# Kernel tuning notes

Hardware: AMD Instinct MI355X
Metric: run time of the kernel (lower is better)

Reference implementation:

```python
import jax, jax.numpy as jnp
import numpy as np

N_USER, N_ITEM, D = 50000, 100000, 64
E_UI, E_UU = 1000000, 800000
NEG_SLOPE = 0.2


def gatv2(x_src, x_dst, src_idx, dst_idx, w_src, w_dst, attn, bias, n_dst):
    """DGL GATv2Conv, num_heads=1: e = a . leaky_relu(Ws x_u + Wd x_v),
    segment-softmax over edges incoming to each dst node, message = Ws x_u."""
    hs = x_src @ w_src                      # [Ns, D]
    hd = x_dst @ w_dst                      # [Nd, D]
    pre = jax.nn.leaky_relu(hs[src_idx] + hd[dst_idx], NEG_SLOPE)  # [E, D]
    e = pre @ attn                          # [E]
    emax = jax.ops.segment_max(e, dst_idx, num_segments=n_dst)     # -inf for empty
    a = jnp.exp(e - emax[dst_idx])          # [E]
    denom = jax.ops.segment_sum(a, dst_idx, num_segments=n_dst)    # [Nd]
    num = jax.ops.segment_sum(hs[src_idx] * a[:, None], dst_idx, num_segments=n_dst)
    out = num / jnp.maximum(denom, 1e-9)[:, None]
    return out + bias


def setup_inputs() -> dict:
    key = jax.random.key(0)
    ks = jax.random.split(key, 32)
    s = 1.0 / np.sqrt(D)
    def W(k):
        return jax.random.normal(k, (D, D), jnp.float32) * s
    inp = {
        "h_user": jax.random.normal(ks[0], (N_USER, D), jnp.float32),
        "h_item": jax.random.normal(ks[1], (N_ITEM, D), jnp.float32),
        "rate_src": jax.random.randint(ks[2], (E_UI,), 0, N_USER, jnp.int32),
        "rate_dst": jax.random.randint(ks[3], (E_UI,), 0, N_ITEM, jnp.int32),
        "rb_src": jax.random.randint(ks[4], (E_UI,), 0, N_ITEM, jnp.int32),
        "rb_dst": jax.random.randint(ks[5], (E_UI,), 0, N_USER, jnp.int32),
        "link_src": jax.random.randint(ks[6], (E_UU,), 0, N_USER, jnp.int32),
        "link_dst": jax.random.randint(ks[7], (E_UU,), 0, N_USER, jnp.int32),
    }
    names = ["r1", "rb1", "rb2", "l2"]
    for i, nm in enumerate(names):
        inp[f"w_src_{nm}"] = W(ks[8 + 4 * i])
        inp[f"w_dst_{nm}"] = W(ks[9 + 4 * i])
        inp[f"a_{nm}"] = jax.random.normal(ks[10 + 4 * i], (D,), jnp.float32) * s
        inp[f"b_{nm}"] = jnp.zeros((D,), jnp.float32)
    inp["w_out"] = jax.random.normal(ks[24], (2 * D, D), jnp.float32) * (1.0 / np.sqrt(2 * D))
    inp["b_out"] = jnp.zeros((D,), jnp.float32)
    return inp


def reference(h_user, h_item,
              w_src_r1, w_dst_r1, a_r1, b_r1,
              w_src_rb1, w_dst_rb1, a_rb1, b_rb1,
              w_src_rb2, w_dst_rb2, a_rb2, b_rb2,
              w_src_l2, w_dst_l2, a_l2, b_l2,
              w_out, b_out,
              rate_src, rate_dst, rb_src, rb_dst, link_src, link_dst):
    # layer1 'rate': user -> item
    h1_item = gatv2(h_user, h_item, rate_src, rate_dst,
                    w_src_r1, w_dst_r1, a_r1, b_r1, N_ITEM)
    # layer1 'rated-by': item -> user
    h2_user = gatv2(h_item, h_user, rb_src, rb_dst,
                    w_src_rb1, w_dst_rb1, a_rb1, b_rb1, N_USER)
    # layer2 'rated-by': item(h1) -> user
    infl_user = gatv2(h1_item, h_user, rb_src, rb_dst,
                      w_src_rb2, w_dst_rb2, a_rb2, b_rb2, N_USER)
    # layer2 'link': user(h2) -> user
    social_user = gatv2(h2_user, h_user, link_src, link_dst,
                        w_src_l2, w_dst_l2, a_l2, b_l2, N_USER)
    out = jnp.concatenate([infl_user, social_user], axis=1) @ w_out + b_out
    return out
```

## Files before the change

kernel.cpp:

```cpp
#include <hip/hip_runtime.h>
#include <hip/hip_fp16.h>
#include <math.h>

#define N_USER 50000
#define N_ITEM 100000
#define E_UI   1000000
#define E_UU   800000
#define E_TOT  (E_UI + E_UI + E_UU)
#define NEG_SLOPE 0.2f
#define LOG2E 1.4426950408889634f

#define NB0 391
#define NB1 196
#define NB2 196
#define NBTOT (NB0 + NB1 + NB2)
#define GPB 256
#define MATN (NBTOT * 256)
#define NBP  ((MATN + 1023) / 1024)

#define XS_STRIDE 68

typedef _Float16 h2v __attribute__((ext_vector_type(2)));

#if defined(__has_builtin)
#if __has_builtin(__builtin_amdgcn_fdot2)
#define HAS_FDOT2 1
#endif
#if __has_builtin(__builtin_elementwise_max)
#define HAS_EW_MAX 1
#endif
#if __has_builtin(__builtin_amdgcn_exp2f)
#define HAS_EXP2 1
#endif
#endif

__device__ __forceinline__ float fexp2(float x) {
#ifdef HAS_EXP2
  return __builtin_amdgcn_exp2f(x);
#else
  return exp2f(x);
#endif
}

__device__ __forceinline__ float fdot2acc(__half2 a, __half2 b, float c) {
#ifdef HAS_FDOT2
  return __builtin_amdgcn_fdot2(__builtin_bit_cast(h2v, a), __builtin_bit_cast(h2v, b), c, false);
#else
  float2 af = __half22float2(a), bf = __half22float2(b);
  return fmaf(af.x, bf.x, fmaf(af.y, bf.y, c));
#endif
}

__device__ __forceinline__ __half2 h2max(__half2 a, __half2 b) {
  h2v av = __builtin_bit_cast(h2v, a), bv = __builtin_bit_cast(h2v, b);
#ifdef HAS_EW_MAX
  h2v r = __builtin_elementwise_max(av, bv);
#else
  h2v r; r.x = av.x > bv.x ? av.x : bv.x; r.y = av.y > bv.y ? av.y : bv.y;
#endif
  return __builtin_bit_cast(__half2, r);
}

__device__ __forceinline__ __half2 h2min(__half2 a, __half2 b) {
  h2v av = __builtin_bit_cast(h2v, a), bv = __builtin_bit_cast(h2v, b);
#ifdef HAS_EW_MAX
  h2v r = __builtin_elementwise_min(av, bv);
#else
  h2v r; r.x = av.x < bv.x ? av.x : bv.x; r.y = av.y < bv.y ? av.y : bv.y;
#endif
  return __builtin_bit_cast(__half2, r);
}


__global__ __launch_bounds__(256) void bucket_hist(const int* __restrict__ d0, const int* __restrict__ d1,
                                                   const int* __restrict__ d2, int* __restrict__ mat) {
  int gid = blockIdx.x >> 8;
  int g   = blockIdx.x & 255;
  const int* dst = gid == 0 ? d0 : (gid == 1 ? d1 : d2);
  int E    = (gid == 2) ? E_UU : E_UI;
  int NB   = (gid == 0) ? NB0 : NB1;
  int boff = (gid == 0) ? 0 : (gid == 1 ? NB0 : NB0 + NB1);
  __shared__ int cnt[NB0];
  for (int b = threadIdx.x; b < NB; b += 256) cnt[b] = 0;
  __syncthreads();
  int chunk = (E + 255) >> 8;
  int lo = g * chunk, hi = min(lo + chunk, E);
  for (int i = lo + threadIdx.x; i < hi; i += 256)
    atomicAdd(&cnt[dst[i] >> 8], 1);
  __syncthreads();
  for (int b = threadIdx.x; b < NB; b += 256)
    mat[(boff + b) * 256 + g] = cnt[b];
}


__global__ __launch_bounds__(256) void partial_kernel(const int* __restrict__ counts, int n,
                                                      int* __restrict__ partials) {
  int t = threadIdx.x;
  int base = blockIdx.x * 1024 + t * 4;
  int s = 0;
  if (base + 3 < n) {
    int4 v = *(const int4*)(counts + base);
    s = v.x + v.y + v.z + v.w;
  } else {
    for (int i = base; i < n && i < base + 4; ++i) s += counts[i];
  }
  #pragma unroll
  for (int off = 1; off < 64; off <<= 1) s += __shfl_xor(s, off);
  __shared__ int ws[4];
  if ((t & 63) == 0) ws[t >> 6] = s;
  __syncthreads();
  if (t == 0) partials[blockIdx.x] = ws[0] + ws[1] + ws[2] + ws[3];
}

__global__ __launch_bounds__(256) void scan_apply_fused(const int* __restrict__ counts, int n,
                                                        const int* __restrict__ partials, int nbp,
                                                        int* __restrict__ outp) {
  __shared__ int sp[256];
  int t = threadIdx.x;
  sp[t] = (t < nbp) ? partials[t] : 0;
  __syncthreads();
  for (int off = 1; off < 256; off <<= 1) {
    int v = (t >= off) ? sp[t - off] : 0;
    __syncthreads();
    sp[t] += v;
    __syncthreads();
  }
  int block_off = (blockIdx.x == 0) ? 0 : sp[blockIdx.x - 1];

  int base = blockIdx.x * 1024 + t * 4;
  int4 v = make_int4(0, 0, 0, 0);
  if (base + 3 < n) {
    v = *(const int4*)(counts + base);
  } else {
    int* pv = &v.x;
    for (int i = 0; i < 4; ++i) if (base + i < n) pv[i] = counts[base + i];
  }
  int s = v.x + v.y + v.z + v.w;
  int lane = t & 63;
  int wv = t >> 6;
  int inc = s;
  #pragma unroll
  for (int off = 1; off < 64; off <<= 1) {
    int u = __shfl_up(inc, off);
    if (lane >= off) inc += u;
  }
  __shared__ int wsum[4];
  if (lane == 63) wsum[wv] = inc;
  __syncthreads();
  int woff = 0;
  for (int i = 0; i < wv; ++i) woff += wsum[i];
  int excl = woff + (inc - s) + block_off;
  int4 rp;
  rp.x = excl;
  rp.y = rp.x + v.x;
  rp.z = rp.y + v.y;
  rp.w = rp.z + v.z;
  if (base + 3 < n) {
    *(int4*)(outp + base) = rp;
  } else {
    int* pr = &rp.x;
    for (int i = 0; i < 4; ++i) if (base + i < n) outp[base + i] = pr[i];
  }
}


__global__ __launch_bounds__(256) void bucket_scatter(const int* __restrict__ s0v, const int* __restrict__ d0,
                                                      const int* __restrict__ s1v, const int* __restrict__ d1,
                                                      const int* __restrict__ s2v, const int* __restrict__ d2,
                                                      const int* __restrict__ mscan, unsigned int* __restrict__ pairs) {
  int gid = blockIdx.x >> 8;
  int g   = blockIdx.x & 255;
  const int* src = gid == 0 ? s0v : (gid == 1 ? s1v : s2v);
  const int* dst = gid == 0 ? d0  : (gid == 1 ? d1  : d2);
  int E    = (gid == 2) ? E_UU : E_UI;
  int NB   = (gid == 0) ? NB0 : NB1;
  int boff = (gid == 0) ? 0 : (gid == 1 ? NB0 : NB0 + NB1);
  __shared__ int cur[NB0];
  for (int b = threadIdx.x; b < NB; b += 256) cur[b] = mscan[(boff + b) * 256 + g];
  __syncthreads();
  int chunk = (E + 255) >> 8;
  int lo = g * chunk, hi = min(lo + chunk, E);
  for (int i = lo + threadIdx.x; i < hi; i += 256) {
    int d = dst[i], s = src[i];
    int pos = atomicAdd(&cur[d >> 8], 1);
    pairs[pos] = ((unsigned)(d & 255) << 24) | (unsigned)s;
  }
}


__global__ __launch_bounds__(256) void bucket_finalize(const unsigned int* __restrict__ pairs,
                                                       const int* __restrict__ mscan,
                                                       int* __restrict__ rp, int* __restrict__ col) {
  int gb = blockIdx.x;
  int t  = threadIdx.x;
  int gid  = (gb < NB0) ? 0 : (gb < NB0 + NB1 ? 1 : 2);
  int boff = (gid == 0) ? 0 : (gid == 1 ? NB0 : NB0 + NB1);
  int node_goff = (gid == 0) ? 0 : (gid == 1 ? N_ITEM : N_ITEM + N_USER);
  int n    = (gid == 0) ? N_ITEM : N_USER;
  int b_local = gb - boff;
  int bs = mscan[gb * 256];
  int be = (gb + 1 < NBTOT) ? mscan[(gb + 1) * 256] : E_TOT;

  __shared__ int cnt[256];
  __shared__ int curb[256];
  __shared__ int wsum[4];
  cnt[t] = 0;
  __syncthreads();
  for (int i = bs + t; i < be; i += 256)
    atomicAdd(&cnt[pairs[i] >> 24], 1);
  __syncthreads();

  int v = cnt[t];
  int lane = t & 63, wv = t >> 6;
  int inc = v;
  #pragma unroll
  for (int off = 1; off < 64; off <<= 1) {
    int u = __shfl_up(inc, off);
    if (lane >= off) inc += u;
  }
  if (lane == 63) wsum[wv] = inc;
  __syncthreads();
  int woff = 0;
  for (int i = 0; i < wv; ++i) woff += wsum[i];
  int base = bs + woff + (inc - v);

  int node_local = b_local * 256 + t;
  if (node_local < n) rp[node_goff + node_local] = base;
  if (gb == NBTOT - 1 && t == 255) rp[N_ITEM + 2 * N_USER] = E_TOT;
  curb[t] = base;
  __syncthreads();

  for (int i = bs + t; i < be; i += 256) {
    unsigned u = pairs[i];
    int p = atomicAdd(&curb[u >> 24], 1);
    col[p] = (int)(u & 0xFFFFFFu);
  }
}


__device__ __forceinline__ void load_xtile(const float* __restrict__ X, float* Xs, int base, int N) {
  #pragma unroll
  for (int i = 0; i < 4; ++i) {
    int idx = threadIdx.x * 4 + i * 1024;
    int row = idx >> 6, colc = idx & 63;
    int grow = base + row;
    const float* src = X + (size_t)(grow < N ? grow : N - 1) * 64 + colc;
    *(float4*)(Xs + row * XS_STRIDE + colc) = *(const float4*)src;
  }
}

__device__ __forceinline__ void gemm_phase(const float* __restrict__ Wsrc, float* Ws,
                                           const float* x0, const float* x1,
                                           const float* x2, const float* x3, int c4,
                                           float4& acc0, float4& acc1, float4& acc2, float4& acc3) {
  __syncthreads();
  #pragma unroll
  for (int i = 0; i < 4; ++i) {
    int idx = threadIdx.x * 4 + i * 1024;
    *(float4*)(Ws + idx) = *(const float4*)(Wsrc + idx);
  }
  __syncthreads();
  acc0 = make_float4(0.f, 0.f, 0.f, 0.f);
  acc1 = acc0; acc2 = acc0; acc3 = acc0;
  #pragma unroll 4
  for (int k4 = 0; k4 < 64; k4 += 4) {
    float4 xa = *(const float4*)(x0 + k4);
    float4 xb = *(const float4*)(x1 + k4);
    float4 xc = *(const float4*)(x2 + k4);
    float4 xd = *(const float4*)(x3 + k4);
    #pragma unroll
    for (int kk = 0; kk < 4; ++kk) {
      float4 w = *(const float4*)(Ws + (k4 + kk) * 64 + c4);
      float sa = (&xa.x)[kk], sb = (&xb.x)[kk], sc = (&xc.x)[kk], sd = (&xd.x)[kk];
      acc0.x = fmaf(sa, w.x, acc0.x); acc0.y = fmaf(sa, w.y, acc0.y);
      acc0.z = fmaf(sa, w.z, acc0.z); acc0.w = fmaf(sa, w.w, acc0.w);
      acc1.x = fmaf(sb, w.x, acc1.x); acc1.y = fmaf(sb, w.y, acc1.y);
      acc1.z = fmaf(sb, w.z, acc1.z); acc1.w = fmaf(sb, w.w, acc1.w);
      acc2.x = fmaf(sc, w.x, acc2.x); acc2.y = fmaf(sc, w.y, acc2.y);
      acc2.z = fmaf(sc, w.z, acc2.z); acc2.w = fmaf(sc, w.w, acc2.w);
      acc3.x = fmaf(sd, w.x, acc3.x); acc3.y = fmaf(sd, w.y, acc3.y);
      acc3.z = fmaf(sd, w.z, acc3.z); acc3.w = fmaf(sd, w.w, acc3.w);
    }
  }
}

__device__ __forceinline__ void store4_f32(float* __restrict__ Y, int r0, int r1, int r2, int r3,
                                           int N, int c4,
                                           const float4& a0, const float4& a1,
                                           const float4& a2, const float4& a3) {
  if (r0 < N) *(float4*)(Y + (size_t)r0 * 64 + c4) = a0;
  if (r1 < N) *(float4*)(Y + (size_t)r1 * 64 + c4) = a1;
  if (r2 < N) *(float4*)(Y + (size_t)r2 * 64 + c4) = a2;
  if (r3 < N) *(float4*)(Y + (size_t)r3 * 64 + c4) = a3;
}

__device__ __forceinline__ void store4_f16(__half* __restrict__ Y, int r0, int r1, int r2, int r3,
                                           int N, int c4,
                                           const float4& a0, const float4& a1,
                                           const float4& a2, const float4& a3) {
  uint2 st;
  if (r0 < N) {
    st.x = __builtin_bit_cast(unsigned int, __floats2half2_rn(a0.x, a0.y));
    st.y = __builtin_bit_cast(unsigned int, __floats2half2_rn(a0.z, a0.w));
    *(uint2*)(Y + (size_t)r0 * 64 + c4) = st;
  }
  if (r1 < N) {
    st.x = __builtin_bit_cast(unsigned int, __floats2half2_rn(a1.x, a1.y));
    st.y = __builtin_bit_cast(unsigned int, __floats2half2_rn(a1.z, a1.w));
    *(uint2*)(Y + (size_t)r1 * 64 + c4) = st;
  }
  if (r2 < N) {
    st.x = __builtin_bit_cast(unsigned int, __floats2half2_rn(a2.x, a2.y));
    st.y = __builtin_bit_cast(unsigned int, __floats2half2_rn(a2.z, a2.w));
    *(uint2*)(Y + (size_t)r2 * 64 + c4) = st;
  }
  if (r3 < N) {
    st.x = __builtin_bit_cast(unsigned int, __floats2half2_rn(a3.x, a3.y));
    st.y = __builtin_bit_cast(unsigned int, __floats2half2_rn(a3.z, a3.w));
    *(uint2*)(Y + (size_t)r3 * 64 + c4) = st;
  }
}

__global__ __launch_bounds__(256) void gemm_user4(const float* __restrict__ X,
                                                  const float* __restrict__ W0, const float* __restrict__ W1,
                                                  const float* __restrict__ W2, const float* __restrict__ W3,
                                                  __half* __restrict__ Y0h, float* __restrict__ Y1,
                                                  float* __restrict__ Y2, float* __restrict__ Y3, int N) {
  __shared__ float Xs[64 * XS_STRIDE];
  __shared__ float Ws[64 * 64];
  int base = blockIdx.x * 64;
  load_xtile(X, Xs, base, N);
  int c4 = (threadIdx.x & 15) * 4;
  int rl = threadIdx.x >> 4;
  int r0 = base + rl, r1 = r0 + 16, r2 = r0 + 32, r3 = r0 + 48;
  const float* x0 = Xs + (rl +  0) * XS_STRIDE;
  const float* x1 = Xs + (rl + 16) * XS_STRIDE;
  const float* x2 = Xs + (rl + 32) * XS_STRIDE;
  const float* x3 = Xs + (rl + 48) * XS_STRIDE;
  float4 a0, a1, a2, a3;
  gemm_phase(W0, Ws, x0, x1, x2, x3, c4, a0, a1, a2, a3);
  store4_f16(Y0h, r0, r1, r2, r3, N, c4, a0, a1, a2, a3);
  gemm_phase(W1, Ws, x0, x1, x2, x3, c4, a0, a1, a2, a3);
  store4_f32(Y1, r0, r1, r2, r3, N, c4, a0, a1, a2, a3);
  gemm_phase(W2, Ws, x0, x1, x2, x3, c4, a0, a1, a2, a3);
  store4_f32(Y2, r0, r1, r2, r3, N, c4, a0, a1, a2, a3);
  gemm_phase(W3, Ws, x0, x1, x2, x3, c4, a0, a1, a2, a3);
  store4_f32(Y3, r0, r1, r2, r3, N, c4, a0, a1, a2, a3);
}

__global__ __launch_bounds__(256) void gemm_item2(const float* __restrict__ X,
                                                  const float* __restrict__ W0, const float* __restrict__ W1,
                                                  float* __restrict__ Y0, __half* __restrict__ Y1h, int N) {
  __shared__ float Xs[64 * XS_STRIDE];
  __shared__ float Ws[64 * 64];
  int base = blockIdx.x * 64;
  load_xtile(X, Xs, base, N);
  int c4 = (threadIdx.x & 15) * 4;
  int rl = threadIdx.x >> 4;
  int r0 = base + rl, r1 = r0 + 16, r2 = r0 + 32, r3 = r0 + 48;
  const float* x0 = Xs + (rl +  0) * XS_STRIDE;
  const float* x1 = Xs + (rl + 16) * XS_STRIDE;
  const float* x2 = Xs + (rl + 32) * XS_STRIDE;
  const float* x3 = Xs + (rl + 48) * XS_STRIDE;
  float4 a0, a1, a2, a3;
  gemm_phase(W0, Ws, x0, x1, x2, x3, c4, a0, a1, a2, a3);
  store4_f32(Y0, r0, r1, r2, r3, N, c4, a0, a1, a2, a3);
  gemm_phase(W1, Ws, x0, x1, x2, x3, c4, a0, a1, a2, a3);
  store4_f16(Y1h, r0, r1, r2, r3, N, c4, a0, a1, a2, a3);
}

__global__ __launch_bounds__(256) void gemm_mid2x(const float* __restrict__ XA, const float* __restrict__ WA,
                                                  __half* __restrict__ YA, int NA, int nbA,
                                                  const float* __restrict__ XB, const float* __restrict__ WB,
                                                  __half* __restrict__ YB, int NB_) {
  __shared__ float Ws[64 * 64];
  const float* X; const float* W; __half* Y; int N; int base;
  if ((int)blockIdx.x < nbA) {
    X = XA; W = WA; Y = YA; N = NA; base = blockIdx.x * 64;
  } else {
    X = XB; W = WB; Y = YB; N = NB_; base = (blockIdx.x - nbA) * 64;
  }
  int c4 = (threadIdx.x & 15) * 4;
  int rl = threadIdx.x >> 4;
  int r0 = base + rl, r1 = r0 + 16, r2 = r0 + 32, r3 = r0 + 48;
  const float* x0 = X + (size_t)(r0 < N ? r0 : N - 1) * 64;
  const float* x1 = X + (size_t)(r1 < N ? r1 : N - 1) * 64;
  const float* x2 = X + (size_t)(r2 < N ? r2 : N - 1) * 64;
  const float* x3 = X + (size_t)(r3 < N ? r3 : N - 1) * 64;
  float4 a0, a1, a2, a3;
  gemm_phase(W, Ws, x0, x1, x2, x3, c4, a0, a1, a2, a3);
  store4_f16(Y, r0, r1, r2, r3, N, c4, a0, a1, a2, a3);
}


__global__ __launch_bounds__(256) void gat8n_kernel(
    const __half* __restrict__ hsA, const float* __restrict__ hdAp,
    const int* __restrict__ rpA, const float* __restrict__ attnA, const float* __restrict__ biasA,
    float* __restrict__ outA, int NdA,
    const __half* __restrict__ hsB, const float* __restrict__ hdBp,
    const int* __restrict__ rpB, const float* __restrict__ attnB, const float* __restrict__ biasB,
    float* __restrict__ outB, int NdB,
    const int* __restrict__ col) {
  int w = (blockIdx.x * blockDim.x + threadIdx.x) >> 6;
  int grp = (threadIdx.x >> 3) & 7;
  int q   = threadIdx.x & 7;
  int node = w * 8 + grp;
  bool valid = node < NdA + NdB;
  bool inA = node < NdA;
  const __half* hs  = inA ? hsA  : hsB;
  const float* hd   = inA ? hdAp : hdBp;
  const int* rp     = inA ? rpA  : rpB;
  const float* attn = inA ? attnA : attnB;
  const float* bias = inA ? biasA : biasB;
  float* outp       = inA ? outA : outB;
  int nn = inA ? node : node - NdA;
  if (!valid) nn = 0;
  int s0 = valid ? rp[nn] : 0;
  int s1 = valid ? rp[nn + 1] : 0;

  const __half2 C02 = __floats2half2_rn(NEG_SLOPE, NEG_SLOPE);
  const __half2 Z   = __floats2half2_rn(0.f, 0.f);

  __half2 hd2[4], a2[4];
  {
    const float* hp = hd + (size_t)nn * 64 + q * 8;
    #pragma unroll
    for (int i = 0; i < 2; ++i) {
      float4 v = *(const float4*)(hp + i * 4);
      hd2[2 * i]     = __floats2half2_rn(v.x, v.y);
      hd2[2 * i + 1] = __floats2half2_rn(v.z, v.w);
    }
    const float* ap = attn + q * 8;
    #pragma unroll
    for (int i = 0; i < 2; ++i) {
      float4 v = *(const float4*)(ap + i * 4);
      a2[2 * i]     = __floats2half2_rn(v.x * LOG2E, v.y * LOG2E);
      a2[2 * i + 1] = __floats2half2_rn(v.z * LOG2E, v.w * LOG2E);
    }
  }

  float m = -1e30f, den = 0.f;
  float num[8];
  #pragma unroll
  for (int i = 0; i < 8; ++i) num[i] = 0.f;

  for (int e = s0; e < s1; e += 4) {
    bool h1 = (e + 1) < s1, h2c = (e + 2) < s1, h3 = (e + 3) < s1;
    int sa = col[e];
    int sb = col[h1 ? e + 1 : e];
    int sc = col[h2c ? e + 2 : e];
    int sd = col[h3 ? e + 3 : e];
    uint4 ra = *(const uint4*)(hs + (size_t)sa * 64 + q * 8);
    uint4 rb = *(const uint4*)(hs + (size_t)sb * 64 + q * 8);
    uint4 rc = *(const uint4*)(hs + (size_t)sc * 64 + q * 8);
    uint4 rd = *(const uint4*)(hs + (size_t)sd * 64 + q * 8);
    unsigned rau[4] = {ra.x, ra.y, ra.z, ra.w};
    unsigned rbu[4] = {rb.x, rb.y, rb.z, rb.w};
    unsigned rcu[4] = {rc.x, rc.y, rc.z, rc.w};
    unsigned rdu[4] = {rd.x, rd.y, rd.z, rd.w};

    float ta = 0.f, tb = 0.f, tc = 0.f, td = 0.f;
    #pragma unroll
    for (int i = 0; i < 4; ++i) {
      __half2 xa = __hadd2(__builtin_bit_cast(__half2, rau[i]), hd2[i]);
      ta = fdot2acc(a2[i], __hfma2(C02, h2min(xa, Z), h2max(xa, Z)), ta);
      __half2 xb = __hadd2(__builtin_bit_cast(__half2, rbu[i]), hd2[i]);
      tb = fdot2acc(a2[i], __hfma2(C02, h2min(xb, Z), h2max(xb, Z)), tb);
      __half2 xc = __hadd2(__builtin_bit_cast(__half2, rcu[i]), hd2[i]);
      tc = fdot2acc(a2[i], __hfma2(C02, h2min(xc, Z), h2max(xc, Z)), tc);
      __half2 xd = __hadd2(__builtin_bit_cast(__half2, rdu[i]), hd2[i]);
      td = fdot2acc(a2[i], __hfma2(C02, h2min(xd, Z), h2max(xd, Z)), td);
    }
    #pragma unroll
    for (int off = 1; off < 8; off <<= 1) {
      ta += __shfl_xor(ta, off);
      tb += __shfl_xor(tb, off);
      tc += __shfl_xor(tc, off);
      td += __shfl_xor(td, off);
    }
    if (!h1)  tb = -1e30f;
    if (!h2c) tc = -1e30f;
    if (!h3)  td = -1e30f;

    float tp = fmaxf(fmaxf(ta, tb), fmaxf(tc, td));
    float dd = tp - m;
    if (dd > 11.5f) {
      float sc0 = fexp2(-dd);
      den *= sc0;
      #pragma unroll
      for (int i = 0; i < 8; ++i) num[i] *= sc0;
      m = tp;
    }
    float pa = fexp2(ta - m);
    float pb = fexp2(tb - m);
    float pc = fexp2(tc - m);
    float pd = fexp2(td - m);
    den += (pa + pb) + (pc + pd);
    __half2 pab = __floats2half2_rn(pa, pb);
    __half2 pcd = __floats2half2_rn(pc, pd);

    #pragma unroll
    for (int i = 0; i < 4; ++i) {
      unsigned lo_ab = (rau[i] & 0xFFFFu) | (rbu[i] << 16);
      unsigned hi_ab = (rau[i] >> 16) | (rbu[i] & 0xFFFF0000u);
      unsigned lo_cd = (rcu[i] & 0xFFFFu) | (rdu[i] << 16);
      unsigned hi_cd = (rcu[i] >> 16) | (rdu[i] & 0xFFFF0000u);
      num[2 * i]     = fdot2acc(__builtin_bit_cast(__half2, lo_cd), pcd,
                       fdot2acc(__builtin_bit_cast(__half2, lo_ab), pab, num[2 * i]));
      num[2 * i + 1] = fdot2acc(__builtin_bit_cast(__half2, hi_cd), pcd,
                       fdot2acc(__builtin_bit_cast(__half2, hi_ab), pab, num[2 * i + 1]));
    }
  }

  if (valid) {
    float inv = 1.f / fmaxf(den, 1e-9f);
    const float* bp = bias + q * 8;
    float* op = outp + (size_t)nn * 64 + q * 8;
    #pragma unroll
    for (int i = 0; i < 2; ++i) {
      float4 b4 = *(const float4*)(bp + i * 4);
      float4 o;
      o.x = fmaf(num[4 * i + 0], inv, b4.x);
      o.y = fmaf(num[4 * i + 1], inv, b4.y);
      o.z = fmaf(num[4 * i + 2], inv, b4.z);
      o.w = fmaf(num[4 * i + 3], inv, b4.w);
      *(float4*)(op + i * 4) = o;
    }
  }
}


__global__ __launch_bounds__(256) void final_kernel(const float* __restrict__ A, const float* __restrict__ B,
                                                    const float* __restrict__ W, const float* __restrict__ bias,
                                                    float* __restrict__ Y, int N) {
  __shared__ float Ws[128 * 64];
  #pragma unroll
  for (int i = 0; i < 8; ++i) {
    int idx = threadIdx.x * 4 + i * 1024;
    *(float4*)(Ws + idx) = *(const float4*)(W + idx);
  }
  __syncthreads();
  int c4 = (threadIdx.x & 15) * 4;
  int rl = threadIdx.x >> 4;
  int base = blockIdx.x * 64;

  float4 b4 = *(const float4*)(bias + c4);

  #pragma unroll
  for (int rr = 0; rr < 4; ++rr) {
    int row = base + rr * 16 + rl;
    if (row >= N) continue;
    const float* ar = A + (size_t)row * 64;
    const float* br = B + (size_t)row * 64;
    float4 acc = b4;
    #pragma unroll 4
    for (int k4 = 0; k4 < 64; k4 += 4) {
      float4 xa = *(const float4*)(ar + k4);
      float4 xb = *(const float4*)(br + k4);
      #pragma unroll
      for (int kk = 0; kk < 4; ++kk) {
        float4 wa = *(const float4*)(Ws + (k4 + kk) * 64 + c4);
        float4 wb = *(const float4*)(Ws + (64 + k4 + kk) * 64 + c4);
        float xsa = (&xa.x)[kk], xsb = (&xb.x)[kk];
        acc.x = fmaf(xsa, wa.x, acc.x); acc.x = fmaf(xsb, wb.x, acc.x);
        acc.y = fmaf(xsa, wa.y, acc.y); acc.y = fmaf(xsb, wb.y, acc.y);
        acc.z = fmaf(xsa, wa.z, acc.z); acc.z = fmaf(xsb, wb.z, acc.z);
        acc.w = fmaf(xsa, wa.w, acc.w); acc.w = fmaf(xsb, wb.w, acc.w);
      }
    }
    *(float4*)(Y + (size_t)row * 64 + c4) = acc;
  }
}


extern "C" void kernel_launch(void* const* d_in, const int* in_sizes, int n_in,
                              void* d_out, int out_size, void* d_ws, size_t ws_size,
                              hipStream_t stream) {
  const float* h_user   = (const float*)d_in[0];
  const float* h_item   = (const float*)d_in[1];
  const int* rate_src   = (const int*)d_in[2];
  const int* rate_dst   = (const int*)d_in[3];
  const int* rb_src     = (const int*)d_in[4];
  const int* rb_dst     = (const int*)d_in[5];
  const int* link_src   = (const int*)d_in[6];
  const int* link_dst   = (const int*)d_in[7];
  const float* w_src_r1  = (const float*)d_in[8];
  const float* w_dst_r1  = (const float*)d_in[9];
  const float* a_r1      = (const float*)d_in[10];
  const float* b_r1      = (const float*)d_in[11];
  const float* w_src_rb1 = (const float*)d_in[12];
  const float* w_dst_rb1 = (const float*)d_in[13];
  const float* a_rb1     = (const float*)d_in[14];
  const float* b_rb1     = (const float*)d_in[15];
  const float* w_src_rb2 = (const float*)d_in[16];
  const float* w_dst_rb2 = (const float*)d_in[17];
  const float* a_rb2     = (const float*)d_in[18];
  const float* b_rb2     = (const float*)d_in[19];
  const float* w_src_l2  = (const float*)d_in[20];
  const float* w_dst_l2  = (const float*)d_in[21];
  const float* a_l2      = (const float*)d_in[22];
  const float* b_l2      = (const float*)d_in[23];
  const float* w_out     = (const float*)d_in[24];
  const float* b_out     = (const float*)d_in[25];
  float* out = (float*)d_out;

  char* ws = (char*)d_ws;
  size_t off = 0;
  auto alloc = [&](size_t bytes) -> void* {
    void* p = ws + off;
    off += (bytes + 255) & ~(size_t)255;
    return p;
  };

  float* u1 = (float*)alloc((size_t)N_USER * 64 * 4);
  float* u2 = (float*)alloc((size_t)N_USER * 64 * 4);
  float* u3 = (float*)alloc((size_t)N_USER * 64 * 4);
  float* i0 = (float*)alloc((size_t)N_ITEM * 64 * 4);
  __half* uh0 = (__half*)alloc((size_t)N_USER * 64 * 2);
  __half* ih1 = (__half*)alloc((size_t)N_ITEM * 64 * 2);

  int* mat     = (int*)alloc((size_t)MATN * 4);
  int* mscan   = (int*)alloc((size_t)MATN * 4);
  int* partials= (int*)alloc(256 * 4);
  int* grp     = (int*)alloc((size_t)(N_ITEM + 2 * N_USER + 1) * 4);
  unsigned int* pairs = (unsigned int*)alloc((size_t)E_TOT * 4);
  int* col_all = (int*)alloc((size_t)E_TOT * 4);

  bucket_hist<<<3 * GPB, 256, 0, stream>>>(rate_dst, rb_dst, link_dst, mat);
  partial_kernel<<<NBP, 256, 0, stream>>>(mat, MATN, partials);
  scan_apply_fused<<<NBP, 256, 0, stream>>>(mat, MATN, partials, NBP, mscan);
  bucket_scatter<<<3 * GPB, 256, 0, stream>>>(rate_src, rate_dst, rb_src, rb_dst,
                                              link_src, link_dst, mscan, pairs);
  bucket_finalize<<<NBTOT, 256, 0, stream>>>(pairs, mscan, grp, col_all);

  int* rp_rate = grp;
  int* rp_rb   = grp + N_ITEM;
  int* rp_link = grp + N_ITEM + N_USER;

  gemm_user4<<<(N_USER + 63) / 64, 256, 0, stream>>>(
      h_user, w_src_r1, w_dst_rb1, w_dst_rb2, w_dst_l2, uh0, u1, u2, u3, N_USER);
  gemm_item2<<<(N_ITEM + 63) / 64, 256, 0, stream>>>(
      h_item, w_dst_r1, w_src_rb1, i0, ih1, N_ITEM);

  {
    int nodes = N_ITEM + N_USER;
    gat8n_kernel<<<(nodes + 31) / 32, 256, 0, stream>>>(
        uh0, i0, rp_rate, a_r1,  b_r1,  i0, N_ITEM,
        ih1, u1, rp_rb,   a_rb1, b_rb1, u1, N_USER,
        col_all);
  }

  {
    int nbA = (N_ITEM + 63) / 64;
    int nbB = (N_USER + 63) / 64;
    gemm_mid2x<<<nbA + nbB, 256, 0, stream>>>(
        i0, w_src_rb2, ih1, N_ITEM, nbA,
        u1, w_src_l2,  uh0, N_USER);
  }

  {
    int nodes = N_USER + N_USER;
    gat8n_kernel<<<(nodes + 31) / 32, 256, 0, stream>>>(
        ih1, u2, rp_rb,   a_rb2, b_rb2, u2, N_USER,
        uh0, u3, rp_link, a_l2,  b_l2,  u3, N_USER,
        col_all);
  }

  final_kernel<<<(N_USER + 63) / 64, 256, 0, stream>>>(u2, u3, w_out, b_out, out, N_USER);
}
```

Before: 263.8 us.

## Store all intermediate projections and GAT outputs in fp16

Switches the dst projections (u1,u2,u3,i0) and the GAT layer outputs from fp32 to fp16 storage. The mid GEMM and final GEMM now read half inputs and convert them in registers, and the GAT kernel loads hd as packed halves instead of converting per node. This roughly halves the memory traffic for these intermediates, at the cost of reduced precision in attention logits and layer outputs.

```diff
diff --git a/kernel.cpp b/kernel.cpp
--- a/kernel.cpp
+++ b/kernel.cpp
@@ -284,14 +284,51 @@
   }
 }
 
-__device__ __forceinline__ void store4_f32(float* __restrict__ Y, int r0, int r1, int r2, int r3,
-                                           int N, int c4,
-                                           const float4& a0, const float4& a1,
-                                           const float4& a2, const float4& a3) {
-  if (r0 < N) *(float4*)(Y + (size_t)r0 * 64 + c4) = a0;
-  if (r1 < N) *(float4*)(Y + (size_t)r1 * 64 + c4) = a1;
-  if (r2 < N) *(float4*)(Y + (size_t)r2 * 64 + c4) = a2;
-  if (r3 < N) *(float4*)(Y + (size_t)r3 * 64 + c4) = a3;
+__device__ __forceinline__ void gemm_phase_h(const float* __restrict__ Wsrc, float* Ws,
+                                             const __half* x0, const __half* x1,
+                                             const __half* x2, const __half* x3, int c4,
+                                             float4& acc0, float4& acc1, float4& acc2, float4& acc3) {
+  __syncthreads();
+  #pragma unroll
+  for (int i = 0; i < 4; ++i) {
+    int idx = threadIdx.x * 4 + i * 1024;
+    *(float4*)(Ws + idx) = *(const float4*)(Wsrc + idx);
+  }
+  __syncthreads();
+  acc0 = make_float4(0.f, 0.f, 0.f, 0.f);
+  acc1 = acc0; acc2 = acc0; acc3 = acc0;
+  #pragma unroll 4
+  for (int k4 = 0; k4 < 64; k4 += 4) {
+    uint2 ua = *(const uint2*)(x0 + k4);
+    uint2 ub = *(const uint2*)(x1 + k4);
+    uint2 uc = *(const uint2*)(x2 + k4);
+    uint2 ud = *(const uint2*)(x3 + k4);
+    float2 fa0 = __half22float2(__builtin_bit_cast(__half2, ua.x));
+    float2 fa1 = __half22float2(__builtin_bit_cast(__half2, ua.y));
+    float2 fb0 = __half22float2(__builtin_bit_cast(__half2, ub.x));
+    float2 fb1 = __half22float2(__builtin_bit_cast(__half2, ub.y));
+    float2 fc0 = __half22float2(__builtin_bit_cast(__half2, uc.x));
+    float2 fc1 = __half22float2(__builtin_bit_cast(__half2, uc.y));
+    float2 fd0 = __half22float2(__builtin_bit_cast(__half2, ud.x));
+    float2 fd1 = __half22float2(__builtin_bit_cast(__half2, ud.y));
+    float xav[4] = {fa0.x, fa0.y, fa1.x, fa1.y};
+    float xbv[4] = {fb0.x, fb0.y, fb1.x, fb1.y};
+    float xcv[4] = {fc0.x, fc0.y, fc1.x, fc1.y};
+    float xdv[4] = {fd0.x, fd0.y, fd1.x, fd1.y};
+    #pragma unroll
+    for (int kk = 0; kk < 4; ++kk) {
+      float4 w = *(const float4*)(Ws + (k4 + kk) * 64 + c4);
+      float sa = xav[kk], sb = xbv[kk], sc = xcv[kk], sd = xdv[kk];
+      acc0.x = fmaf(sa, w.x, acc0.x); acc0.y = fmaf(sa, w.y, acc0.y);
+      acc0.z = fmaf(sa, w.z, acc0.z); acc0.w = fmaf(sa, w.w, acc0.w);
+      acc1.x = fmaf(sb, w.x, acc1.x); acc1.y = fmaf(sb, w.y, acc1.y);
+      acc1.z = fmaf(sb, w.z, acc1.z); acc1.w = fmaf(sb, w.w, acc1.w);
+      acc2.x = fmaf(sc, w.x, acc2.x); acc2.y = fmaf(sc, w.y, acc2.y);
+      acc2.z = fmaf(sc, w.z, acc2.z); acc2.w = fmaf(sc, w.w, acc2.w);
+      acc3.x = fmaf(sd, w.x, acc3.x); acc3.y = fmaf(sd, w.y, acc3.y);
+      acc3.z = fmaf(sd, w.z, acc3.z); acc3.w = fmaf(sd, w.w, acc3.w);
+    }
+  }
 }
 
 __device__ __forceinline__ void store4_f16(__half* __restrict__ Y, int r0, int r1, int r2, int r3,
@@ -324,8 +361,8 @@
 __global__ __launch_bounds__(256) void gemm_user4(const float* __restrict__ X,
                                                   const float* __restrict__ W0, const float* __restrict__ W1,
                                                   const float* __restrict__ W2, const float* __restrict__ W3,
-                                                  __half* __restrict__ Y0h, float* __restrict__ Y1,
-                                                  float* __restrict__ Y2, float* __restrict__ Y3, int N) {
+                                                  __half* __restrict__ Y0, __half* __restrict__ Y1,
+                                                  __half* __restrict__ Y2, __half* __restrict__ Y3, int N) {
   __shared__ float Xs[64 * XS_STRIDE];
   __shared__ float Ws[64 * 64];
   int base = blockIdx.x * 64;
@@ -339,18 +376,18 @@
   const float* x3 = Xs + (rl + 48) * XS_STRIDE;
   float4 a0, a1, a2, a3;
   gemm_phase(W0, Ws, x0, x1, x2, x3, c4, a0, a1, a2, a3);
-  store4_f16(Y0h, r0, r1, r2, r3, N, c4, a0, a1, a2, a3);
+  store4_f16(Y0, r0, r1, r2, r3, N, c4, a0, a1, a2, a3);
   gemm_phase(W1, Ws, x0, x1, x2, x3, c4, a0, a1, a2, a3);
-  store4_f32(Y1, r0, r1, r2, r3, N, c4, a0, a1, a2, a3);
+  store4_f16(Y1, r0, r1, r2, r3, N, c4, a0, a1, a2, a3);
   gemm_phase(W2, Ws, x0, x1, x2, x3, c4, a0, a1, a2, a3);
-  store4_f32(Y2, r0, r1, r2, r3, N, c4, a0, a1, a2, a3);
+  store4_f16(Y2, r0, r1, r2, r3, N, c4, a0, a1, a2, a3);
   gemm_phase(W3, Ws, x0, x1, x2, x3, c4, a0, a1, a2, a3);
-  store4_f32(Y3, r0, r1, r2, r3, N, c4, a0, a1, a2, a3);
+  store4_f16(Y3, r0, r1, r2, r3, N, c4, a0, a1, a2, a3);
 }
 
 __global__ __launch_bounds__(256) void gemm_item2(const float* __restrict__ X,
                                                   const float* __restrict__ W0, const float* __restrict__ W1,
-                                                  float* __restrict__ Y0, __half* __restrict__ Y1h, int N) {
+                                                  __half* __restrict__ Y0, __half* __restrict__ Y1, int N) {
   __shared__ float Xs[64 * XS_STRIDE];
   __shared__ float Ws[64 * 64];
   int base = blockIdx.x * 64;
@@ -364,17 +401,17 @@
   const float* x3 = Xs + (rl + 48) * XS_STRIDE;
   float4 a0, a1, a2, a3;
   gemm_phase(W0, Ws, x0, x1, x2, x3, c4, a0, a1, a2, a3);
-  store4_f32(Y0, r0, r1, r2, r3, N, c4, a0, a1, a2, a3);
+  store4_f16(Y0, r0, r1, r2, r3, N, c4, a0, a1, a2, a3);
   gemm_phase(W1, Ws, x0, x1, x2, x3, c4, a0, a1, a2, a3);
-  store4_f16(Y1h, r0, r1, r2, r3, N, c4, a0, a1, a2, a3);
-}
-
-__global__ __launch_bounds__(256) void gemm_mid2x(const float* __restrict__ XA, const float* __restrict__ WA,
+  store4_f16(Y1, r0, r1, r2, r3, N, c4, a0, a1, a2, a3);
+}
+
+__global__ __launch_bounds__(256) void gemm_mid2x(const __half* __restrict__ XA, const float* __restrict__ WA,
                                                   __half* __restrict__ YA, int NA, int nbA,
-                                                  const float* __restrict__ XB, const float* __restrict__ WB,
+                                                  const __half* __restrict__ XB, const float* __restrict__ WB,
                                                   __half* __restrict__ YB, int NB_) {
   __shared__ float Ws[64 * 64];
-  const float* X; const float* W; __half* Y; int N; int base;
+  const __half* X; const float* W; __half* Y; int N; int base;
   if ((int)blockIdx.x < nbA) {
     X = XA; W = WA; Y = YA; N = NA; base = blockIdx.x * 64;
   } else {
@@ -383,23 +420,23 @@
   int c4 = (threadIdx.x & 15) * 4;
   int rl = threadIdx.x >> 4;
   int r0 = base + rl, r1 = r0 + 16, r2 = r0 + 32, r3 = r0 + 48;
-  const float* x0 = X + (size_t)(r0 < N ? r0 : N - 1) * 64;
-  const float* x1 = X + (size_t)(r1 < N ? r1 : N - 1) * 64;
-  const float* x2 = X + (size_t)(r2 < N ? r2 : N - 1) * 64;
-  const float* x3 = X + (size_t)(r3 < N ? r3 : N - 1) * 64;
+  const __half* x0 = X + (size_t)(r0 < N ? r0 : N - 1) * 64;
+  const __half* x1 = X + (size_t)(r1 < N ? r1 : N - 1) * 64;
+  const __half* x2 = X + (size_t)(r2 < N ? r2 : N - 1) * 64;
+  const __half* x3 = X + (size_t)(r3 < N ? r3 : N - 1) * 64;
   float4 a0, a1, a2, a3;
-  gemm_phase(W, Ws, x0, x1, x2, x3, c4, a0, a1, a2, a3);
+  gemm_phase_h(W, Ws, x0, x1, x2, x3, c4, a0, a1, a2, a3);
   store4_f16(Y, r0, r1, r2, r3, N, c4, a0, a1, a2, a3);
 }
 
 
 __global__ __launch_bounds__(256) void gat8n_kernel(
-    const __half* __restrict__ hsA, const float* __restrict__ hdAp,
+    const __half* __restrict__ hsA, const __half* __restrict__ hdAp,
     const int* __restrict__ rpA, const float* __restrict__ attnA, const float* __restrict__ biasA,
-    float* __restrict__ outA, int NdA,
-    const __half* __restrict__ hsB, const float* __restrict__ hdBp,
+    __half* __restrict__ outA, int NdA,
+    const __half* __restrict__ hsB, const __half* __restrict__ hdBp,
     const int* __restrict__ rpB, const float* __restrict__ attnB, const float* __restrict__ biasB,
-    float* __restrict__ outB, int NdB,
+    __half* __restrict__ outB, int NdB,
     const int* __restrict__ col) {
   int w = (blockIdx.x * blockDim.x + threadIdx.x) >> 6;
   int grp = (threadIdx.x >> 3) & 7;
@@ -408,11 +445,11 @@
   bool valid = node < NdA + NdB;
   bool inA = node < NdA;
   const __half* hs  = inA ? hsA  : hsB;
-  const float* hd   = inA ? hdAp : hdBp;
+  const __half* hd  = inA ? hdAp : hdBp;
   const int* rp     = inA ? rpA  : rpB;
   const float* attn = inA ? attnA : attnB;
   const float* bias = inA ? biasA : biasB;
-  float* outp       = inA ? outA : outB;
+  __half* outp      = inA ? outA : outB;
   int nn = inA ? node : node - NdA;
   if (!valid) nn = 0;
   int s0 = valid ? rp[nn] : 0;
@@ -423,13 +460,11 @@
 
   __half2 hd2[4], a2[4];
   {
-    const float* hp = hd + (size_t)nn * 64 + q * 8;
-    #pragma unroll
-    for (int i = 0; i < 2; ++i) {
-      float4 v = *(const float4*)(hp + i * 4);
-      hd2[2 * i]     = __floats2half2_rn(v.x, v.y);
-      hd2[2 * i + 1] = __floats2half2_rn(v.z, v.w);
-    }
+    uint4 hv = *(const uint4*)(hd + (size_t)nn * 64 + q * 8);
+    hd2[0] = __builtin_bit_cast(__half2, hv.x);
+    hd2[1] = __builtin_bit_cast(__half2, hv.y);
+    hd2[2] = __builtin_bit_cast(__half2, hv.z);
+    hd2[3] = __builtin_bit_cast(__half2, hv.w);
     const float* ap = attn + q * 8;
     #pragma unroll
     for (int i = 0; i < 2; ++i) {
@@ -515,22 +550,23 @@
   if (valid) {
     float inv = 1.f / fmaxf(den, 1e-9f);
     const float* bp = bias + q * 8;
-    float* op = outp + (size_t)nn * 64 + q * 8;
-    #pragma unroll
-    for (int i = 0; i < 2; ++i) {
-      float4 b4 = *(const float4*)(bp + i * 4);
-      float4 o;
-      o.x = fmaf(num[4 * i + 0], inv, b4.x);
-      o.y = fmaf(num[4 * i + 1], inv, b4.y);
-      o.z = fmaf(num[4 * i + 2], inv, b4.z);
-      o.w = fmaf(num[4 * i + 3], inv, b4.w);
-      *(float4*)(op + i * 4) = o;
-    }
-  }
-}
-
-
-__global__ __launch_bounds__(256) void final_kernel(const float* __restrict__ A, const float* __restrict__ B,
+    float4 b0 = *(const float4*)(bp);
+    float4 b1 = *(const float4*)(bp + 4);
+    uint4 st;
+    st.x = __builtin_bit_cast(unsigned int,
+        __floats2half2_rn(fmaf(num[0], inv, b0.x), fmaf(num[1], inv, b0.y)));
+    st.y = __builtin_bit_cast(unsigned int,
+        __floats2half2_rn(fmaf(num[2], inv, b0.z), fmaf(num[3], inv, b0.w)));
+    st.z = __builtin_bit_cast(unsigned int,
+        __floats2half2_rn(fmaf(num[4], inv, b1.x), fmaf(num[5], inv, b1.y)));
+    st.w = __builtin_bit_cast(unsigned int,
+        __floats2half2_rn(fmaf(num[6], inv, b1.z), fmaf(num[7], inv, b1.w)));
+    *(uint4*)(outp + (size_t)nn * 64 + q * 8) = st;
+  }
+}
+
+
+__global__ __launch_bounds__(256) void final_kernel(const __half* __restrict__ A, const __half* __restrict__ B,
                                                     const float* __restrict__ W, const float* __restrict__ bias,
                                                     float* __restrict__ Y, int N) {
   __shared__ float Ws[128 * 64];
@@ -550,18 +586,24 @@
   for (int rr = 0; rr < 4; ++rr) {
     int row = base + rr * 16 + rl;
     if (row >= N) continue;
-    const float* ar = A + (size_t)row * 64;
-    const float* br = B + (size_t)row * 64;
+    const __half* ar = A + (size_t)row * 64;
+    const __half* br = B + (size_t)row * 64;
     float4 acc = b4;
     #pragma unroll 4
     for (int k4 = 0; k4 < 64; k4 += 4) {
-      float4 xa = *(const float4*)(ar + k4);
-      float4 xb = *(const float4*)(br + k4);
+      uint2 ua = *(const uint2*)(ar + k4);
+      uint2 ub = *(const uint2*)(br + k4);
+      float2 fa0 = __half22float2(__builtin_bit_cast(__half2, ua.x));
+      float2 fa1 = __half22float2(__builtin_bit_cast(__half2, ua.y));
+      float2 fb0 = __half22float2(__builtin_bit_cast(__half2, ub.x));
+      float2 fb1 = __half22float2(__builtin_bit_cast(__half2, ub.y));
+      float xav[4] = {fa0.x, fa0.y, fa1.x, fa1.y};
+      float xbv[4] = {fb0.x, fb0.y, fb1.x, fb1.y};
       #pragma unroll
       for (int kk = 0; kk < 4; ++kk) {
         float4 wa = *(const float4*)(Ws + (k4 + kk) * 64 + c4);
         float4 wb = *(const float4*)(Ws + (64 + k4 + kk) * 64 + c4);
-        float xsa = (&xa.x)[kk], xsb = (&xb.x)[kk];
+        float xsa = xav[kk], xsb = xbv[kk];
         acc.x = fmaf(xsa, wa.x, acc.x); acc.x = fmaf(xsb, wb.x, acc.x);
         acc.y = fmaf(xsa, wa.y, acc.y); acc.y = fmaf(xsb, wb.y, acc.y);
         acc.z = fmaf(xsa, wa.z, acc.z); acc.z = fmaf(xsb, wb.z, acc.z);
@@ -612,11 +654,11 @@
     return p;
   };
 
-  float* u1 = (float*)alloc((size_t)N_USER * 64 * 4);
-  float* u2 = (float*)alloc((size_t)N_USER * 64 * 4);
-  float* u3 = (float*)alloc((size_t)N_USER * 64 * 4);
-  float* i0 = (float*)alloc((size_t)N_ITEM * 64 * 4);
   __half* uh0 = (__half*)alloc((size_t)N_USER * 64 * 2);
+  __half* u1  = (__half*)alloc((size_t)N_USER * 64 * 2);
+  __half* u2  = (__half*)alloc((size_t)N_USER * 64 * 2);
+  __half* u3  = (__half*)alloc((size_t)N_USER * 64 * 2);
+  __half* i0  = (__half*)alloc((size_t)N_ITEM * 64 * 2);
   __half* ih1 = (__half*)alloc((size_t)N_ITEM * 64 * 2);
 
   int* mat     = (int*)alloc((size_t)MATN * 4);
```

Measured after the change: 258.3 us. -2.1%, faster.
